# Kernel optimization log

Hardware: AMD Instinct MI355X
Metric: run time of the kernel (lower is better)

Reference implementation:

```python
import jax, jax.numpy as jnp
import numpy as np

B, T, C, H = 2, 2048, 1024, 16
D = C // H  # 64
RW, RA, RG = 64, 64, 128  # decay / a / gate LoRA ranks
EPS = 1e-5


def setup_inputs() -> dict:
    key = jax.random.key(0)
    ks = iter(jax.random.split(key, 40))
    n = lambda s, sc=0.02: jax.random.normal(next(ks), s, jnp.float32) * sc
    u = lambda s: jax.random.uniform(next(ks), s, jnp.float32)
    return dict(
        hidden_states=jax.random.normal(next(ks), (B, T, C), jnp.float32),
        # token-mix (time-shift lerp) params
        x_r=u((C,)), x_w=u((C,)), x_k=u((C,)), x_v=u((C,)), x_a=u((C,)), x_g=u((C,)),
        k_k=u((C,)), k_a=u((C,)), r_k=n((H, D), 0.1),
        # square projections (stored [in, out]; x @ W)
        W_r=n((C, C)), W_k=n((C, C)), W_v=n((C, C)), W_o=n((C, C)),
        # LoRA: out = act(x @ A) @ Bm + bias (activation between the two linears)
        w_lora_a=n((C, RW)), w_lora_b=n((RW, C)), w_lora_bias=n((C,), 0.1),
        a_lora_a=n((C, RA)), a_lora_b=n((RA, C)), a_lora_bias=jnp.zeros((C,), jnp.float32),
        g_lora_a=n((C, RG)), g_lora_b=n((RG, C)), g_lora_bias=jnp.zeros((C,), jnp.float32),
        # GroupNorm(num_heads groups over value_dim)
        gn_weight=jnp.ones((C,), jnp.float32), gn_bias=jnp.zeros((C,), jnp.float32),
    )


def _rwkv7_scan(r, log_w, k, v, a, b):
    # all inputs [B, T, H, D]; state S: [B, H, D_v, D_k]
    # S_t = S_{t-1} * diag(exp(log_w_t)) + (S_{t-1} @ a_t) b_t^T + v_t k_t^T
    # o_t = S_t @ r_t
    Bn, Tn, Hn, Dn = r.shape

    def step(S, xs):
        r_t, w_t, k_t, v_t, a_t, b_t = xs  # each [B, H, D]
        sa = jnp.einsum('bhij,bhj->bhi', S, a_t)          # S @ a (pre-decay state)
        S = (S * jnp.exp(w_t)[:, :, None, :]
             + sa[..., None] * b_t[:, :, None, :]
             + v_t[..., None] * k_t[:, :, None, :])
        o_t = jnp.einsum('bhij,bhj->bhi', S, r_t)
        return S, o_t

    S0 = jnp.zeros((Bn, Hn, Dn, Dn), r.dtype)
    xs = tuple(jnp.swapaxes(x, 0, 1) for x in (r, log_w, k, v, a, b))  # [T,B,H,D]
    _, o = jax.lax.scan(step, S0, xs)
    return jnp.swapaxes(o, 0, 1)  # [B, T, H, D]


def reference(hidden_states, x_r, x_w, x_k, x_v, x_a, x_g, k_k, k_a, r_k,
              W_r, W_k, W_v, W_o,
              w_lora_a, w_lora_b, w_lora_bias,
              a_lora_a, a_lora_b, a_lora_bias,
              g_lora_a, g_lora_b, g_lora_bias,
              gn_weight, gn_bias):
    Bn, Tn, Cn = hidden_states.shape
    # time shift: pad one step of zeros at the front, drop last
    shifted = jnp.concatenate([jnp.zeros_like(hidden_states[:, :1]), hidden_states[:, :-1]], axis=1)
    delta = shifted - hidden_states

    xr = hidden_states + delta * x_r
    xw = hidden_states + delta * x_w
    xk = hidden_states + delta * x_k
    xv = hidden_states + delta * x_v
    xa = hidden_states + delta * x_a

    r = xr @ W_r
    log_w = -jax.nn.softplus(-((jnp.tanh(xw @ w_lora_a) @ w_lora_b) + w_lora_bias)) - 0.5
    k = xk @ W_k
    v = xv @ W_v
    a = jax.nn.sigmoid((xa @ a_lora_a) @ a_lora_b + a_lora_bias)
    # g_lora(r): sigmoid activation sits BETWEEN the two LoRA linears
    g = jax.nn.sigmoid(r @ g_lora_a) @ g_lora_b + g_lora_bias

    kk = (k * k_k).reshape(Bn, Tn, H, D)
    kk = kk / jnp.maximum(jnp.linalg.norm(kk, axis=-1, keepdims=True), 1e-12)  # per-head L2 norm
    k = k * (1.0 + (a - 1.0) * k_a)

    rh = r.reshape(Bn, Tn, H, D)
    wh = log_w.reshape(Bn, Tn, H, D)
    kh = k.reshape(Bn, Tn, H, D)
    vh = v.reshape(Bn, Tn, H, D)
    ah = a.reshape(Bn, Tn, H, D)

    o = _rwkv7_scan(rh, wh, kh, vh, -kk, kk * ah)  # [B, T, H, D]

    # GroupNorm over value_dim with H groups (stats per head)
    mu = o.mean(-1, keepdims=True)
    var = ((o - mu) ** 2).mean(-1, keepdims=True)
    o_flat = ((o - mu) * jax.lax.rsqrt(var + EPS)).reshape(Bn, Tn, C) * gn_weight + gn_bias

    bonus = ((rh * kh * r_k).sum(-1, keepdims=True) * vh).reshape(Bn, Tn, C)
    o_flat = o_flat + bonus
    return (o_flat * g) @ W_o
```

## Files before the change

### kernel.cpp

```cpp
#include <hip/hip_runtime.h>
#include <hip/hip_bf16.h>
#include <hip/hip_fp16.h>
#include <stdint.h>
#include <stddef.h>

typedef __hip_bfloat16 bf16;
typedef _Float16 f16;
typedef __attribute__((ext_vector_type(8))) short short8;
typedef __attribute__((ext_vector_type(8))) _Float16 half8;
typedef __attribute__((ext_vector_type(4))) float f32x4;
typedef __attribute__((ext_vector_type(2))) float f32x2;
typedef unsigned short us;

__device__ __forceinline__ float dsigm(float z){ return 1.f/(1.f+expf(-z)); }

template<int CTRL>
__device__ __forceinline__ float dpp_term(float x) {
  int xi = __builtin_bit_cast(int, x);
  int yi = __builtin_amdgcn_update_dpp(0, xi, CTRL, 0xF, 0xF, false);
  return __builtin_bit_cast(float, yi);
}
__device__ __forceinline__ float red4(float x) {
  x += dpp_term<0xB1>(x);
  x += dpp_term<0x4E>(x);
  return x;
}

__device__ __forceinline__ void split1(float v, us& h, us& l) {
  bf16 hb = __float2bfloat16(v);
  h = __builtin_bit_cast(us, hb);
  float hf = __bfloat162float(hb);
  bf16 lb = __float2bfloat16(v - hf);
  l = __builtin_bit_cast(us, lb);
}

__device__ __forceinline__ void split8(const float* f, short8& h, short8& l) {
#pragma unroll
  for (int e = 0; e < 8; ++e) {
    us hh, ll;
    split1(f[e], hh, ll);
    h[e] = (short)hh; l[e] = (short)ll;
  }
}

__device__ __forceinline__ void gl16(const f16* g, f16* l) {
  __builtin_amdgcn_global_load_lds((const __attribute__((address_space(1))) void*)g,
                                   (__attribute__((address_space(3))) void*)l, 16, 0, 0);
}

__device__ __forceinline__ void emit16(const float* __restrict__ marr, int c4,
    const float4& cur, const float4& dlt, f16* __restrict__ out, int row)
{
  float4 m = *(const float4*)(marr + c4);
  f16* o = out + (size_t)row*1024 + c4;
  o[0] = (f16)fmaf(dlt.x, m.x, cur.x);
  o[1] = (f16)fmaf(dlt.y, m.y, cur.y);
  o[2] = (f16)fmaf(dlt.z, m.z, cur.z);
  o[3] = (f16)fmaf(dlt.w, m.w, cur.w);
}

__global__ void k_prep(const float* __restrict__ hs,
    const float* __restrict__ mr, const float* __restrict__ mw, const float* __restrict__ mk,
    const float* __restrict__ mv, const float* __restrict__ ma,
    f16* __restrict__ oxr, f16* __restrict__ oxw, f16* __restrict__ oxk,
    f16* __restrict__ oxv, f16* __restrict__ oxa)
{
  int id = blockIdx.x * 256 + threadIdx.x;
  int row = id >> 8;
  int c4 = (id & 255) << 2;
  int t = row & 2047;
  const float* hp = hs + (size_t)row*1024 + c4;
  float4 cur = *(const float4*)hp;
  float4 prev = make_float4(0.f,0.f,0.f,0.f);
  if (t > 0) prev = *(const float4*)(hp - 1024);
  float4 dlt = make_float4(prev.x-cur.x, prev.y-cur.y, prev.z-cur.z, prev.w-cur.w);
  emit16(mr, c4, cur, dlt, oxr, row);
  emit16(mw, c4, cur, dlt, oxw, row);
  emit16(mk, c4, cur, dlt, oxk, row);
  emit16(mv, c4, cur, dlt, oxv, row);
  emit16(ma, c4, cur, dlt, oxa, row);
}

struct SrcP { const float* p[10]; };
struct DstP { f16* p[10]; };

__global__ void k_transpose(SrcP S, DstP Dd)
{
  static constexpr int TR[10]  = {1024,1024,1024,1024,1024,  64,1024,  64,1024, 128};
  static constexpr int TCC[10] = {1024,1024,1024,1024,  64,1024,  64,1024, 128,1024};
  static constexpr int TCP[10] = {1024,1024,1024,1024, 128,1024, 128,1024, 128,1024};
  int z = blockIdx.z;
  int R = TR[z], Cc = TCC[z], Cp = TCP[z];
  int n0 = blockIdx.x * 32, r0 = blockIdx.y * 32;
  if (n0 >= Cp || r0 >= R) return;
  const float* src = S.p[z];
  f16* dst = Dd.p[z];
  int tx = threadIdx.x, ty = threadIdx.y;
  __shared__ float tile[32][33];
  if (n0 < Cc) {
#pragma unroll
    for (int i = 0; i < 4; ++i)
      tile[ty + 8*i][tx] = src[(size_t)(r0 + ty + 8*i)*Cc + n0 + tx];
    __syncthreads();
#pragma unroll
    for (int i = 0; i < 4; ++i)
      dst[(size_t)(n0 + ty + 8*i)*R + r0 + tx] = (f16)tile[tx][ty + 8*i];
  } else {
#pragma unroll
    for (int i = 0; i < 4; ++i)
      dst[(size_t)(n0 + ty + 8*i)*R + r0 + tx] = (f16)0.f;
  }
}

struct GJob {
  const f16* A;
  const f16* Bt;
  float* C;
  f16* Cpk;
  const float* bias;
  int K; int N; int Npk; int ldc; int act;
  int lda; int ldb;
};
struct GJobs { GJob j[5]; };

__global__ __launch_bounds__(256) void k_gemm_fp16(GJobs jobs)
{
  GJob jb = jobs.j[blockIdx.z];
  const int colBase = blockIdx.y * 128;
  if (colBase >= jb.N) return;
  const int rowBase = blockIdx.x * 128;
  __shared__ __align__(16) f16 As[128*64];
  __shared__ __align__(16) f16 Bs[128*64];
  const int tid = threadIdx.x;
  const int l = tid & 63, w = tid >> 6;
  const int wm = w >> 1, wn = w & 1;
  const int lrow = l & 15;
  const int nk = jb.K >> 6;

  const f16* Arow[4]; const f16* Brow[4]; int ld[4];
#pragma unroll
  for (int i2 = 0; i2 < 4; ++i2) {
    int s = (i2*4 + w)*64 + l;
    int ar = s >> 3;
    int unit = s & 7;
    int acs = (unit ^ (ar & 7)) * 8;
    Arow[i2] = jb.A  + (size_t)(rowBase + ar)*jb.lda + acs;
    Brow[i2] = jb.Bt + (size_t)(colBase + ar)*jb.ldb + acs;
    ld[i2] = (i2*4 + w) * 512;
  }

  f32x4 acc[4][4];
#pragma unroll
  for (int i = 0; i < 4; ++i)
#pragma unroll
    for (int j = 0; j < 4; ++j) { f32x4 z = {0.f,0.f,0.f,0.f}; acc[i][j] = z; }

  for (int kt = 0; kt < nk; ++kt) {
    const int kh = kt*64;
#pragma unroll
    for (int i2 = 0; i2 < 4; ++i2) {
      gl16(Arow[i2] + kh, &As[ld[i2]]);
      gl16(Brow[i2] + kh, &Bs[ld[i2]]);
    }
    __syncthreads();
#pragma unroll
    for (int ks = 0; ks < 2; ++ks) {
      half8 ah[4], bh[4];
#pragma unroll
      for (int mt = 0; mt < 4; ++mt) {
        int row = wm*64 + mt*16 + lrow;
        int cu = ks*4 + (l >> 4);
        ah[mt] = *(const half8*)&As[row*64 + ((cu ^ (row & 7)) * 8)];
      }
#pragma unroll
      for (int nt = 0; nt < 4; ++nt) {
        int row = wn*64 + nt*16 + lrow;
        int cu = ks*4 + (l >> 4);
        bh[nt] = *(const half8*)&Bs[row*64 + ((cu ^ (row & 7)) * 8)];
      }
#pragma unroll
      for (int mt = 0; mt < 4; ++mt)
#pragma unroll
        for (int nt = 0; nt < 4; ++nt)
          acc[mt][nt] = __builtin_amdgcn_mfma_f32_16x16x32_f16(ah[mt], bh[nt], acc[mt][nt], 0, 0, 0);
    }
    __syncthreads();
  }
#pragma unroll
  for (int mt = 0; mt < 4; ++mt) {
    int row = rowBase + wm*64 + mt*16 + (l >> 4)*4;
#pragma unroll
    for (int nt = 0; nt < 4; ++nt) {
      int col = colBase + wn*64 + nt*16 + (l & 15);
      float bv = (jb.bias != nullptr) ? jb.bias[col] : 0.f;
#pragma unroll
      for (int rg = 0; rg < 4; ++rg) {
        float v = acc[mt][nt][rg] + bv;
        if (jb.act == 1)      v = dsigm(v);
        else if (jb.act == 2) v = tanhf(v);
        else if (jb.act == 3) v = 0.60653066f * dsigm(v);
        if (jb.C) jb.C[(size_t)(row + rg)*jb.ldc + col] = v;
        if (jb.Cpk && col < jb.Npk)
          jb.Cpk[(size_t)(row + rg)*jb.Npk + col] = (f16)v;
      }
    }
  }
}

__global__ void k_scanprep(f16* __restrict__ kA, f16* __restrict__ aA,
                           const float* __restrict__ kkw, const float* __restrict__ kaw,
                           f16* __restrict__ kkA)
{
  int idx = blockIdx.x * 256 + threadIdx.x;
  size_t gt8 = (size_t)idx * 8;
  int ch = (int)(gt8 & 1023);
  half8 k8 = *(const half8*)(kA + gt8);
  half8 a8 = *(const half8*)(aA + gt8);
  float kw[8], ka_[8];
  *(float4*)&kw[0]  = *(const float4*)(kkw + ch);
  *(float4*)&kw[4]  = *(const float4*)(kkw + ch + 4);
  *(float4*)&ka_[0] = *(const float4*)(kaw + ch);
  *(float4*)&ka_[4] = *(const float4*)(kaw + ch + 4);
  float kkv[8]; float ss = 0.f;
#pragma unroll
  for (int e = 0; e < 8; ++e) { kkv[e] = (float)k8[e] * kw[e]; ss += kkv[e]*kkv[e]; }
  ss += __shfl_xor(ss, 1); ss += __shfl_xor(ss, 2); ss += __shfl_xor(ss, 4);
  float inv = 1.f / fmaxf(sqrtf(ss), 1e-12f);
  half8 kkn8, bb8, kup8;
#pragma unroll
  for (int e = 0; e < 8; ++e) {
    float kkn = kkv[e] * inv;
    float av = (float)a8[e];
    kkn8[e] = (f16)kkn;
    bb8[e]  = (f16)(kkn * av);
    kup8[e] = (f16)((float)k8[e] * fmaf(av - 1.f, ka_[e], 1.f));
  }
  *(half8*)(kkA + gt8) = kkn8;
  *(half8*)(aA + gt8)  = bb8;
  *(half8*)(kA + gt8)  = kup8;
}

__device__ __forceinline__ void step_pk16(const float* __restrict__ sb, int s,
    f32x2* u2, f32x2* p2, float* __restrict__ o0A, float* __restrict__ zA,
    size_t base, int i, int q, int j0)
{
  f32x2 kk2[8];
#pragma unroll
  for (int hh = 0; hh < 4; ++hh) {
    float4 a1 = *(const float4*)(sb + 512 + s*64 + j0 + hh*4);
    kk2[hh*2+0] = f32x2{a1.x, a1.y}; kk2[hh*2+1] = f32x2{a1.z, a1.w};
  }
  f32x2 uk2 = u2[0]*kk2[0], pk2 = p2[0]*kk2[0];
#pragma unroll
  for (int e = 1; e < 8; ++e) { uk2 += u2[e]*kk2[e]; pk2 += p2[e]*kk2[e]; }
  float uk = red4(uk2.x + uk2.y);
  float pk = red4(pk2.x + pk2.y);
  float vi = sb[2560 + s*64 + i];
  const f32x2 su2 = {-uk, -uk}, sp2 = {-pk, -pk}, vi2 = {vi, vi};
  f32x2 oo2 = {0.f, 0.f}, zz2 = {0.f, 0.f};
#pragma unroll
  for (int hh = 0; hh < 4; ++hh) {
    float4 e4 = *(const float4*)(sb + 0    + s*64 + j0 + hh*4);
    float4 b4 = *(const float4*)(sb + 1024 + s*64 + j0 + hh*4);
    float4 k4 = *(const float4*)(sb + 1536 + s*64 + j0 + hh*4);
    float4 r4 = *(const float4*)(sb + 2048 + s*64 + j0 + hh*4);
    f32x2 ew0 = {e4.x, e4.y}, ew1 = {e4.z, e4.w};
    f32x2 bb0 = {b4.x, b4.y}, bb1 = {b4.z, b4.w};
    f32x2 kv0 = {k4.x, k4.y}, kv1 = {k4.z, k4.w};
    f32x2 rr0 = {r4.x, r4.y}, rr1 = {r4.z, r4.w};
    int e0 = hh*2, e1 = hh*2 + 1;
    f32x2 uu0 = u2[e0]*ew0 + su2*bb0 + vi2*kv0;
    u2[e0] = uu0; oo2 += uu0*rr0;
    f32x2 pp0 = p2[e0]*ew0 + sp2*bb0;
    p2[e0] = pp0; zz2 += pp0*rr0;
    f32x2 uu1 = u2[e1]*ew1 + su2*bb1 + vi2*kv1;
    u2[e1] = uu1; oo2 += uu1*rr1;
    f32x2 pp1 = p2[e1]*ew1 + sp2*bb1;
    p2[e1] = pp1; zz2 += pp1*rr1;
  }
  float oo = red4(oo2.x + oo2.y);
  float zz = red4(zz2.x + zz2.y);
  if (q == 0) { o0A[base + i] = oo; zA[base + i] = zz; }
}

__global__ __launch_bounds__(256) void k_scan_p1(
    const f16* __restrict__ rA, const f16* __restrict__ ewA,
    const f16* __restrict__ kA, const f16* __restrict__ vA,
    const f16* __restrict__ kkA, const f16* __restrict__ bbA,
    float* __restrict__ o0A, float* __restrict__ zA,
    float* __restrict__ UcA, float* __restrict__ PTcA)
{
  const int blk = blockIdx.x;
  const int bh = blk & 31, c = blk >> 5;
  const int b = bh >> 4, h = bh & 15;
  const int tid = threadIdx.x;
  const int i = tid >> 2, q = tid & 3, j0 = q * 16;
  const size_t base0 = (size_t)b*2048*1024 + (size_t)h*64 + (size_t)(c*64)*1024;

  __shared__ __align__(16) float smem[6144];

  const int aA_ = tid >> 6, rmA = tid & 63, ssA = rmA >> 3, fA = rmA & 7;
  const f16* paA = (aA_==0) ? ewA : (aA_==1) ? kkA : (aA_==2) ? bbA : kA;
  const f16* srcA = paA + base0 + (size_t)ssA*1024 + fA*8;
  const int dstA = aA_*512 + ssA*64 + fA*8;
  const int hasB = (tid < 128);
  const int sB = 256 + tid;
  const int aB_ = sB >> 6, rmB = sB & 63, ssB = rmB >> 3, fB = rmB & 7;
  const f16* paB = (aB_ == 4) ? rA : vA;
  const f16* srcB = paB + base0 + (size_t)ssB*1024 + fB*8;
  const int dstB = aB_*512 + ssB*64 + fB*8;

  f32x2 u2[8], p2[8];
#pragma unroll
  for (int e = 0; e < 8; ++e) {
    u2[e] = f32x2{0.f, 0.f};
    float p0 = (j0 + 2*e     == i) ? 1.f : 0.f;
    float p1 = (j0 + 2*e + 1 == i) ? 1.f : 0.f;
    p2[e] = f32x2{p0, p1};
  }

  {
    half8 hA = *(const half8*)(srcA);
    *(float4*)&smem[dstA]     = make_float4((float)hA[0], (float)hA[1], (float)hA[2], (float)hA[3]);
    *(float4*)&smem[dstA + 4] = make_float4((float)hA[4], (float)hA[5], (float)hA[6], (float)hA[7]);
    if (hasB) {
      half8 hB = *(const half8*)(srcB);
      *(float4*)&smem[dstB]     = make_float4((float)hB[0], (float)hB[1], (float)hB[2], (float)hB[3]);
      *(float4*)&smem[dstB + 4] = make_float4((float)hB[4], (float)hB[5], (float)hB[6], (float)hB[7]);
    }
  }
  __syncthreads();

  int curb = 0;
  for (int g = 0; g < 8; ++g) {
    half8 nA, nB;
    if (g < 7) {
      nA = *(const half8*)(srcA + (size_t)(g+1)*8192);
      if (hasB) nB = *(const half8*)(srcB + (size_t)(g+1)*8192);
    }
    const float* sb = smem + curb*3072;
#pragma unroll
    for (int s = 0; s < 8; ++s)
      step_pk16(sb, s, u2, p2, o0A, zA, base0 + (size_t)(g*8 + s)*1024, i, q, j0);
    if (g < 7) {
      int nb = curb ^ 1;
      *(float4*)&smem[nb*3072 + dstA]     = make_float4((float)nA[0], (float)nA[1], (float)nA[2], (float)nA[3]);
      *(float4*)&smem[nb*3072 + dstA + 4] = make_float4((float)nA[4], (float)nA[5], (float)nA[6], (float)nA[7]);
      if (hasB) {
        *(float4*)&smem[nb*3072 + dstB]     = make_float4((float)nB[0], (float)nB[1], (float)nB[2], (float)nB[3]);
        *(float4*)&smem[nb*3072 + dstB + 4] = make_float4((float)nB[4], (float)nB[5], (float)nB[6], (float)nB[7]);
      }
    }
    __syncthreads();
    curb ^= 1;
  }

  const size_t cbase = ((size_t)(bh*32 + c)) * 4096;
#pragma unroll
  for (int e4 = 0; e4 < 4; ++e4)
    *(float4*)(UcA + cbase + (size_t)i*64 + j0 + e4*4) =
      make_float4(u2[e4*2].x, u2[e4*2].y, u2[e4*2+1].x, u2[e4*2+1].y);
  float (*lds)[65] = (float(*)[65])smem;
#pragma unroll
  for (int e = 0; e < 8; ++e) {
    lds[i][j0 + 2*e]     = p2[e].x;
    lds[i][j0 + 2*e + 1] = p2[e].y;
  }
  __syncthreads();
#pragma unroll
  for (int e4 = 0; e4 < 4; ++e4) {
    float4 wv = make_float4(lds[j0 + e4*4 + 0][i], lds[j0 + e4*4 + 1][i],
                            lds[j0 + e4*4 + 2][i], lds[j0 + e4*4 + 3][i]);
    *(float4*)(PTcA + cbase + (size_t)i*64 + j0 + e4*4) = wv;
  }
}

__device__ __forceinline__ void chain_body(int c, int bh, int w, int lr, int lq,
    float (&Slds)[64][65], f32x4 (&acc)[4],
    float (&u_c)[4][4], float4 (&p_c)[2][2],
    float (&u_n)[4][4], float4 (&p_n)[2][2],
    const float* __restrict__ UcA, const float* __restrict__ PTcA,
    float* __restrict__ S0A)
{
  const size_t s0base = ((size_t)bh*32 + c) * 4096;
#pragma unroll
  for (int mt = 0; mt < 4; ++mt)
#pragma unroll
    for (int rg = 0; rg < 4; ++rg) {
      Slds[mt*16 + lq*4 + rg][w*16 + lr] = acc[mt][rg];
      if (c > 0) S0A[s0base + (size_t)(mt*16 + lq*4 + rg)*64 + w*16 + lr] = acc[mt][rg];
    }
  __syncthreads();
  if (c + 1 < 32) {
    const size_t nbase = ((size_t)bh*32 + c + 1) * 4096;
#pragma unroll
    for (int mt = 0; mt < 4; ++mt)
#pragma unroll
      for (int rg = 0; rg < 4; ++rg)
        u_n[mt][rg] = UcA[nbase + (size_t)(mt*16 + lq*4 + rg)*64 + w*16 + lr];
#pragma unroll
    for (int kt = 0; kt < 2; ++kt)
#pragma unroll
      for (int hh = 0; hh < 2; ++hh)
        p_n[kt][hh] = *(const float4*)(PTcA + nbase + (size_t)(w*16 + lr)*64 + kt*32 + lq*8 + hh*4);
  }
  short8 pbh[2], pbl[2];
#pragma unroll
  for (int kt = 0; kt < 2; ++kt) {
    float f[8] = {p_c[kt][0].x, p_c[kt][0].y, p_c[kt][0].z, p_c[kt][0].w,
                  p_c[kt][1].x, p_c[kt][1].y, p_c[kt][1].z, p_c[kt][1].w};
    split8(f, pbh[kt], pbl[kt]);
  }
  f32x4 nacc[4];
#pragma unroll
  for (int mt = 0; mt < 4; ++mt) {
    f32x4 z = {u_c[mt][0], u_c[mt][1], u_c[mt][2], u_c[mt][3]};
    nacc[mt] = z;
  }
#pragma unroll
  for (int kt = 0; kt < 2; ++kt)
#pragma unroll
    for (int mt = 0; mt < 4; ++mt) {
      float f[8];
#pragma unroll
      for (int e = 0; e < 8; ++e) f[e] = Slds[mt*16 + lr][kt*32 + lq*8 + e];
      short8 sah, sal;
      split8(f, sah, sal);
      nacc[mt] = __builtin_amdgcn_mfma_f32_16x16x32_bf16(sah, pbh[kt], nacc[mt], 0, 0, 0);
      nacc[mt] = __builtin_amdgcn_mfma_f32_16x16x32_bf16(sal, pbh[kt], nacc[mt], 0, 0, 0);
      nacc[mt] = __builtin_amdgcn_mfma_f32_16x16x32_bf16(sah, pbl[kt], nacc[mt], 0, 0, 0);
    }
#pragma unroll
  for (int mt = 0; mt < 4; ++mt) acc[mt] = nacc[mt];
  __syncthreads();
}

__global__ __launch_bounds__(256) void k_chain(
    const float* __restrict__ UcA, const float* __restrict__ PTcA,
    float* __restrict__ S0A)
{
  const int bh = blockIdx.x;
  const int l = threadIdx.x & 63, w = threadIdx.x >> 6;
  const int lr = l & 15, lq = l >> 4;
  __shared__ float Slds[64][65];

  f32x4 acc[4];
#pragma unroll
  for (int mt = 0; mt < 4; ++mt) { f32x4 z = {0.f,0.f,0.f,0.f}; acc[mt] = z; }

  float u0[4][4], u1[4][4];
  float4 p0[2][2], p1[2][2];
  {
    const size_t cbase = (size_t)bh * 32 * 4096;
#pragma unroll
    for (int mt = 0; mt < 4; ++mt)
#pragma unroll
      for (int rg = 0; rg < 4; ++rg)
        u0[mt][rg] = UcA[cbase + (size_t)(mt*16 + lq*4 + rg)*64 + w*16 + lr];
#pragma unroll
    for (int kt = 0; kt < 2; ++kt)
#pragma unroll
      for (int hh = 0; hh < 2; ++hh)
        p0[kt][hh] = *(const float4*)(PTcA + cbase + (size_t)(w*16 + lr)*64 + kt*32 + lq*8 + hh*4);
  }
  for (int c = 0; c < 32; c += 2) {
    chain_body(c,     bh, w, lr, lq, Slds, acc, u0, p0, u1, p1, UcA, PTcA, S0A);
    chain_body(c + 1, bh, w, lr, lq, Slds, acc, u1, p1, u0, p0, UcA, PTcA, S0A);
  }
}

__global__ __launch_bounds__(256) void k_corrpost(
    const float* __restrict__ S0A, const float* __restrict__ zA,
    const float* __restrict__ o0A, const f16* __restrict__ rA,
    const f16* __restrict__ kA, const f16* __restrict__ vA,
    const float* __restrict__ rk, const float* __restrict__ gnw,
    const float* __restrict__ gnb, const f16* __restrict__ gA,
    f16* __restrict__ yH)
{
  const int blk = blockIdx.x;
  const int bh = blk & 31;
  const int c  = blk >> 5;
  const int b = bh >> 4, h = bh & 15;
  const int l = threadIdx.x & 63, w = threadIdx.x >> 6;
  const int lr = l & 15, lq = l >> 4;

  f32x4 a2[4];
#pragma unroll
  for (int nt = 0; nt < 4; ++nt) { f32x4 z = {0.f,0.f,0.f,0.f}; a2[nt] = z; }

  if (c > 0) {
    const size_t s0base = ((size_t)bh*32 + c) * 4096;
    short8 sbh[4][2], sbl[4][2];
#pragma unroll
    for (int nt = 0; nt < 4; ++nt)
#pragma unroll
      for (int kt = 0; kt < 2; ++kt) {
        float f[8];
#pragma unroll
        for (int e = 0; e < 8; ++e)
          f[e] = S0A[s0base + (size_t)(nt*16 + lr)*64 + kt*32 + lq*8 + e];
        split8(f, sbh[nt][kt], sbl[nt][kt]);
      }
    short8 zh[2], zl[2];
#pragma unroll
    for (int kt = 0; kt < 2; ++kt) {
      const float* zp = zA + ((size_t)(b*2048 + c*64 + w*16 + lr)*16 + h)*64 + kt*32 + lq*8;
      float f[8];
#pragma unroll
      for (int e = 0; e < 8; ++e) f[e] = zp[e];
      split8(f, zh[kt], zl[kt]);
    }
#pragma unroll
    for (int kt = 0; kt < 2; ++kt)
#pragma unroll
      for (int nt = 0; nt < 4; ++nt) {
        a2[nt] = __builtin_amdgcn_mfma_f32_16x16x32_bf16(zh[kt], sbh[nt][kt], a2[nt], 0, 0, 0);
        a2[nt] = __builtin_amdgcn_mfma_f32_16x16x32_bf16(zl[kt], sbh[nt][kt], a2[nt], 0, 0, 0);
        a2[nt] = __builtin_amdgcn_mfma_f32_16x16x32_bf16(zh[kt], sbl[nt][kt], a2[nt], 0, 0, 0);
      }
  }

#pragma unroll
  for (int rg = 0; rg < 4; ++rg) {
    const int tl = w*16 + lq*4 + rg;
    const size_t trow = (size_t)(b*2048 + c*64 + tl);
    const size_t rb = trow*1024 + h*64;
    float o4[4], v4[4];
    float sum = 0.f, pr = 0.f;
#pragma unroll
    for (int nt = 0; nt < 4; ++nt) {
      const int ii = nt*16 + lr;
      float o = o0A[rb + ii] + a2[nt][rg];
      o4[nt] = o; sum += o;
      v4[nt] = (float)vA[rb + ii];
      pr += (float)rA[rb + ii] * (float)kA[rb + ii] * rk[h*64 + ii];
    }
    sum += __shfl_xor(sum,1); sum += __shfl_xor(sum,2);
    sum += __shfl_xor(sum,4); sum += __shfl_xor(sum,8);
    pr  += __shfl_xor(pr,1);  pr  += __shfl_xor(pr,2);
    pr  += __shfl_xor(pr,4);  pr  += __shfl_xor(pr,8);
    float mean = sum * (1.f/64.f);
    float vp = 0.f;
#pragma unroll
    for (int nt = 0; nt < 4; ++nt) { float d = o4[nt]-mean; vp += d*d; }
    vp += __shfl_xor(vp,1); vp += __shfl_xor(vp,2);
    vp += __shfl_xor(vp,4); vp += __shfl_xor(vp,8);
    float inv = rsqrtf(vp*(1.f/64.f) + 1e-5f);
#pragma unroll
    for (int nt = 0; nt < 4; ++nt) {
      const int ii = nt*16 + lr;
      const int ch = h*64 + ii;
      float y = (o4[nt]-mean)*inv*gnw[ch] + gnb[ch];
      y = fmaf(pr, v4[nt], y);
      y *= (float)gA[rb + ii];
      yH[trow*1024 + ch] = (f16)y;
    }
  }
}

extern "C" void kernel_launch(void* const* d_in, const int* in_sizes, int n_in,
                              void* d_out, int out_size, void* d_ws, size_t ws_size,
                              hipStream_t stream)
{
  (void)in_sizes; (void)n_in; (void)out_size; (void)ws_size;
  const float* hs     = (const float*)d_in[0];
  const float* x_r    = (const float*)d_in[1];
  const float* x_w    = (const float*)d_in[2];
  const float* x_k    = (const float*)d_in[3];
  const float* x_v    = (const float*)d_in[4];
  const float* x_a    = (const float*)d_in[5];
  const float* k_k    = (const float*)d_in[7];
  const float* k_a    = (const float*)d_in[8];
  const float* r_k    = (const float*)d_in[9];
  const float* W_r    = (const float*)d_in[10];
  const float* W_k    = (const float*)d_in[11];
  const float* W_v    = (const float*)d_in[12];
  const float* W_o    = (const float*)d_in[13];
  const float* wla    = (const float*)d_in[14];
  const float* wlb    = (const float*)d_in[15];
  const float* wlbias = (const float*)d_in[16];
  const float* ala    = (const float*)d_in[17];
  const float* alb    = (const float*)d_in[18];
  const float* albias = (const float*)d_in[19];
  const float* gla    = (const float*)d_in[20];
  const float* glb    = (const float*)d_in[21];
  const float* glbias = (const float*)d_in[22];
  const float* gnw    = (const float*)d_in[23];
  const float* gnb    = (const float*)d_in[24];

  char* ws = (char*)d_ws;
  size_t cur = 0;
  auto take = [&](size_t bytes) { size_t o = cur; cur += (bytes + 255) & ~(size_t)255; return o; };

  f16* xr_h = (f16*)(ws + take((size_t)4096*1024*2));
  f16* xw_h = (f16*)(ws + take((size_t)4096*1024*2));
  f16* xk_h = (f16*)(ws + take((size_t)4096*1024*2));
  f16* xv_h = (f16*)(ws + take((size_t)4096*1024*2));
  f16* xa_h = (f16*)(ws + take((size_t)4096*1024*2));
  f16* Wr_p  = (f16*)(ws + take((size_t)1024*1024*2));
  f16* Wk_p  = (f16*)(ws + take((size_t)1024*1024*2));
  f16* Wv_p  = (f16*)(ws + take((size_t)1024*1024*2));
  f16* Wo_p  = (f16*)(ws + take((size_t)1024*1024*2));
  f16* wla_p = (f16*)(ws + take((size_t)128*1024*2));
  f16* wlb_p = (f16*)(ws + take((size_t)1024*64*2));
  f16* ala_p = (f16*)(ws + take((size_t)128*1024*2));
  f16* alb_p = (f16*)(ws + take((size_t)1024*64*2));
  f16* gla_p = (f16*)(ws + take((size_t)128*1024*2));
  f16* glb_p = (f16*)(ws + take((size_t)1024*128*2));
  f16* r_h  = (f16*)(ws + take((size_t)4096*1024*2));
  f16* k_h  = (f16*)(ws + take((size_t)4096*1024*2));
  f16* v_h  = (f16*)(ws + take((size_t)4096*1024*2));
  f16* kk_h = (f16*)(ws + take((size_t)4096*1024*2));
  f16* g_h  = (f16*)(ws + take((size_t)4096*1024*2));
  f16* t2w  = (f16*)(ws + take((size_t)4096*64*2));
  f16* t2a  = (f16*)(ws + take((size_t)4096*64*2));
  f16* t2g  = (f16*)(ws + take((size_t)4096*128*2));
  float* z_f  = (float*)(ws + take((size_t)4096*1024*4));
  float* Uc_f = (float*)(ws + take((size_t)4096*1024*4));
  float* PT_f = (float*)(ws + take((size_t)4096*1024*4));
  f16*   ew_h = xw_h;
  f16*   a_h  = xa_h;
  f16*   y_h  = xr_h;
  float* S0_f = (float*)xk_h;
  float* oF   = (float*)d_out;

  k_prep<<<4096, 256, 0, stream>>>(hs, x_r, x_w, x_k, x_v, x_a,
                                   xr_h, xw_h, xk_h, xv_h, xa_h);
  SrcP sp; DstP dp;
  sp.p[0]=W_r; sp.p[1]=W_k; sp.p[2]=W_v; sp.p[3]=W_o;
  sp.p[4]=wla; sp.p[5]=wlb; sp.p[6]=ala; sp.p[7]=alb; sp.p[8]=gla; sp.p[9]=glb;
  dp.p[0]=Wr_p; dp.p[1]=Wk_p; dp.p[2]=Wv_p; dp.p[3]=Wo_p;
  dp.p[4]=wla_p; dp.p[5]=wlb_p; dp.p[6]=ala_p; dp.p[7]=alb_p; dp.p[8]=gla_p; dp.p[9]=glb_p;
  k_transpose<<<dim3(32,32,10), dim3(32,8), 0, stream>>>(sp, dp);

  GJobs J{};
  auto job = [](const f16* A, const f16* Bt, float* C, f16* Cpk, const float* bias,
                int K, int N, int Npk, int ldc, int act, int lda, int ldb) {
    GJob j; j.A=A; j.Bt=Bt; j.C=C; j.Cpk=Cpk; j.bias=bias;
    j.K=K; j.N=N; j.Npk=Npk; j.ldc=ldc; j.act=act; j.lda=lda; j.ldb=ldb;
    return j;
  };

  J.j[0] = job(xr_h, Wr_p,  nullptr, r_h, nullptr, 1024, 1024, 1024, 0, 0, 1024, 1024);
  J.j[1] = job(xk_h, Wk_p,  nullptr, k_h, nullptr, 1024, 1024, 1024, 0, 0, 1024, 1024);
  J.j[2] = job(xv_h, Wv_p,  nullptr, v_h, nullptr, 1024, 1024, 1024, 0, 0, 1024, 1024);
  J.j[3] = job(xw_h, wla_p, nullptr, t2w, nullptr, 1024, 128,  64,   0, 2, 1024, 1024);
  J.j[4] = job(xa_h, ala_p, nullptr, t2a, nullptr, 1024, 128,  64,   0, 0, 1024, 1024);
  k_gemm_fp16<<<dim3(32,8,5), 256, 0, stream>>>(J);

  J = GJobs{};
  J.j[0] = job(t2w, wlb_p, nullptr, ew_h, wlbias, 64,   1024, 1024, 0, 3, 64,   64);
  J.j[1] = job(t2a, alb_p, nullptr, a_h,  albias, 64,   1024, 1024, 0, 1, 64,   64);
  J.j[2] = job(r_h, gla_p, nullptr, t2g,  nullptr, 1024, 128,  128,  0, 1, 1024, 1024);
  k_gemm_fp16<<<dim3(32,8,3), 256, 0, stream>>>(J);

  J = GJobs{};
  J.j[0] = job(t2g, glb_p, nullptr, g_h, glbias, 128, 1024, 1024, 0, 0, 128, 128);
  k_gemm_fp16<<<dim3(32,8,1), 256, 0, stream>>>(J);

  k_scanprep<<<2048, 256, 0, stream>>>(k_h, a_h, k_k, k_a, kk_h);

  k_scan_p1<<<1024, 256, 0, stream>>>(r_h, ew_h, k_h, v_h, kk_h, a_h, oF, z_f, Uc_f, PT_f);
  k_chain<<<32, 256, 0, stream>>>(Uc_f, PT_f, S0_f);

  k_corrpost<<<1024, 256, 0, stream>>>(S0_f, z_f, oF, r_h, k_h, v_h,
                                       r_k, gnw, gnb, g_h, y_h);

  J = GJobs{};
  J.j[0] = job(y_h, Wo_p, (float*)d_out, nullptr, nullptr, 1024, 1024, 0, 1024, 0, 1024, 1024);
  k_gemm_fp16<<<dim3(32,8,1), 256, 0, stream>>>(J);
}
```

Before: 315.4 us.

## Split chunk scan into separate U and P state blocks for more parallelism

The first-phase chunked scan kernel used to advance both the zero-init state U and the identity-init transition P in one block. It now launches twice as many blocks, each advancing only one of the two recurrences, with smaller staged tiles of 4 timesteps and a smaller shared-memory footprint. The aim is more concurrent blocks and fewer registers per thread, which improves occupancy and latency hiding on the serial recurrence. The cost is that shared inputs (ew, kk, bb, r) are loaded twice, and there are more sync rounds per chunk.

```diff
diff --git a/kernel.cpp b/kernel.cpp
--- a/kernel.cpp
+++ b/kernel.cpp
@@ -240,30 +240,28 @@
   *(half8*)(kA + gt8)  = kup8;
 }
 
-__device__ __forceinline__ void step_pk16(const float* __restrict__ sb, int s,
-    f32x2* u2, f32x2* p2, float* __restrict__ o0A, float* __restrict__ zA,
-    size_t base, int i, int q, int j0)
+__device__ __forceinline__ void step_U(const float* __restrict__ sb, int s,
+    f32x2* u2, float* __restrict__ o0A, size_t base, int i, int q, int j0)
 {
   f32x2 kk2[8];
 #pragma unroll
   for (int hh = 0; hh < 4; ++hh) {
-    float4 a1 = *(const float4*)(sb + 512 + s*64 + j0 + hh*4);
+    float4 a1 = *(const float4*)(sb + 256 + s*64 + j0 + hh*4);
     kk2[hh*2+0] = f32x2{a1.x, a1.y}; kk2[hh*2+1] = f32x2{a1.z, a1.w};
   }
-  f32x2 uk2 = u2[0]*kk2[0], pk2 = p2[0]*kk2[0];
-#pragma unroll
-  for (int e = 1; e < 8; ++e) { uk2 += u2[e]*kk2[e]; pk2 += p2[e]*kk2[e]; }
+  f32x2 uk2 = u2[0]*kk2[0];
+#pragma unroll
+  for (int e = 1; e < 8; ++e) uk2 += u2[e]*kk2[e];
   float uk = red4(uk2.x + uk2.y);
-  float pk = red4(pk2.x + pk2.y);
-  float vi = sb[2560 + s*64 + i];
-  const f32x2 su2 = {-uk, -uk}, sp2 = {-pk, -pk}, vi2 = {vi, vi};
-  f32x2 oo2 = {0.f, 0.f}, zz2 = {0.f, 0.f};
+  float vi = sb[1280 + s*64 + i];
+  const f32x2 su2 = {-uk, -uk}, vi2 = {vi, vi};
+  f32x2 oo2 = {0.f, 0.f};
 #pragma unroll
   for (int hh = 0; hh < 4; ++hh) {
     float4 e4 = *(const float4*)(sb + 0    + s*64 + j0 + hh*4);
-    float4 b4 = *(const float4*)(sb + 1024 + s*64 + j0 + hh*4);
-    float4 k4 = *(const float4*)(sb + 1536 + s*64 + j0 + hh*4);
-    float4 r4 = *(const float4*)(sb + 2048 + s*64 + j0 + hh*4);
+    float4 b4 = *(const float4*)(sb + 512  + s*64 + j0 + hh*4);
+    float4 k4 = *(const float4*)(sb + 768  + s*64 + j0 + hh*4);
+    float4 r4 = *(const float4*)(sb + 1024 + s*64 + j0 + hh*4);
     f32x2 ew0 = {e4.x, e4.y}, ew1 = {e4.z, e4.w};
     f32x2 bb0 = {b4.x, b4.y}, bb1 = {b4.z, b4.w};
     f32x2 kv0 = {k4.x, k4.y}, kv1 = {k4.z, k4.w};
@@ -271,16 +269,44 @@
     int e0 = hh*2, e1 = hh*2 + 1;
     f32x2 uu0 = u2[e0]*ew0 + su2*bb0 + vi2*kv0;
     u2[e0] = uu0; oo2 += uu0*rr0;
+    f32x2 uu1 = u2[e1]*ew1 + su2*bb1 + vi2*kv1;
+    u2[e1] = uu1; oo2 += uu1*rr1;
+  }
+  float oo = red4(oo2.x + oo2.y);
+  if (q == 0) o0A[base + i] = oo;
+}
+
+__device__ __forceinline__ void step_P(const float* __restrict__ sb, int s,
+    f32x2* p2, float* __restrict__ zA, size_t base, int i, int q, int j0)
+{
+  f32x2 kk2[8];
+#pragma unroll
+  for (int hh = 0; hh < 4; ++hh) {
+    float4 a1 = *(const float4*)(sb + 256 + s*64 + j0 + hh*4);
+    kk2[hh*2+0] = f32x2{a1.x, a1.y}; kk2[hh*2+1] = f32x2{a1.z, a1.w};
+  }
+  f32x2 pk2 = p2[0]*kk2[0];
+#pragma unroll
+  for (int e = 1; e < 8; ++e) pk2 += p2[e]*kk2[e];
+  float pk = red4(pk2.x + pk2.y);
+  const f32x2 sp2 = {-pk, -pk};
+  f32x2 zz2 = {0.f, 0.f};
+#pragma unroll
+  for (int hh = 0; hh < 4; ++hh) {
+    float4 e4 = *(const float4*)(sb + 0   + s*64 + j0 + hh*4);
+    float4 b4 = *(const float4*)(sb + 512 + s*64 + j0 + hh*4);
+    float4 r4 = *(const float4*)(sb + 768 + s*64 + j0 + hh*4);
+    f32x2 ew0 = {e4.x, e4.y}, ew1 = {e4.z, e4.w};
+    f32x2 bb0 = {b4.x, b4.y}, bb1 = {b4.z, b4.w};
+    f32x2 rr0 = {r4.x, r4.y}, rr1 = {r4.z, r4.w};
+    int e0 = hh*2, e1 = hh*2 + 1;
     f32x2 pp0 = p2[e0]*ew0 + sp2*bb0;
     p2[e0] = pp0; zz2 += pp0*rr0;
-    f32x2 uu1 = u2[e1]*ew1 + su2*bb1 + vi2*kv1;
-    u2[e1] = uu1; oo2 += uu1*rr1;
     f32x2 pp1 = p2[e1]*ew1 + sp2*bb1;
     p2[e1] = pp1; zz2 += pp1*rr1;
   }
-  float oo = red4(oo2.x + oo2.y);
   float zz = red4(zz2.x + zz2.y);
-  if (q == 0) { o0A[base + i] = oo; zA[base + i] = zz; }
+  if (q == 0) zA[base + i] = zz;
 }
 
 __global__ __launch_bounds__(256) void k_scan_p1(
@@ -291,87 +317,89 @@
     float* __restrict__ UcA, float* __restrict__ PTcA)
 {
   const int blk = blockIdx.x;
-  const int bh = blk & 31, c = blk >> 5;
+  const int role = blk >> 10;
+  const int idx = blk & 1023;
+  const int bh = idx & 31, c = idx >> 5;
   const int b = bh >> 4, h = bh & 15;
   const int tid = threadIdx.x;
   const int i = tid >> 2, q = tid & 3, j0 = q * 16;
   const size_t base0 = (size_t)b*2048*1024 + (size_t)h*64 + (size_t)(c*64)*1024;
 
-  __shared__ __align__(16) float smem[6144];
-
-  const int aA_ = tid >> 6, rmA = tid & 63, ssA = rmA >> 3, fA = rmA & 7;
-  const f16* paA = (aA_==0) ? ewA : (aA_==1) ? kkA : (aA_==2) ? bbA : kA;
-  const f16* srcA = paA + base0 + (size_t)ssA*1024 + fA*8;
-  const int dstA = aA_*512 + ssA*64 + fA*8;
-  const int hasB = (tid < 128);
-  const int sB = 256 + tid;
-  const int aB_ = sB >> 6, rmB = sB & 63, ssB = rmB >> 3, fB = rmB & 7;
-  const f16* paB = (aB_ == 4) ? rA : vA;
-  const f16* srcB = paB + base0 + (size_t)ssB*1024 + fB*8;
-  const int dstB = aB_*512 + ssB*64 + fB*8;
-
-  f32x2 u2[8], p2[8];
+  __shared__ __align__(16) float smem[4160];
+
+  const int nslots = role ? 128 : 192;
+  const int a0 = tid >> 5, rm = tid & 31, s0 = rm >> 3, f0 = rm & 7;
+  const f16* pa;
+  if (role == 0)
+    pa = (a0==0) ? ewA : (a0==1) ? kkA : (a0==2) ? bbA :
+         (a0==3) ? kA  : (a0==4) ? rA  : vA;
+  else
+    pa = (a0==0) ? ewA : (a0==1) ? kkA : (a0==2) ? bbA : rA;
+  const int active = (tid < nslots);
+  const f16* src0 = pa + base0 + (size_t)s0*1024 + f0*8;
+  const int dst0 = a0*256 + s0*64 + f0*8;
+
+  f32x2 st[8];
 #pragma unroll
   for (int e = 0; e < 8; ++e) {
-    u2[e] = f32x2{0.f, 0.f};
-    float p0 = (j0 + 2*e     == i) ? 1.f : 0.f;
-    float p1 = (j0 + 2*e + 1 == i) ? 1.f : 0.f;
-    p2[e] = f32x2{p0, p1};
-  }
-
-  {
-    half8 hA = *(const half8*)(srcA);
-    *(float4*)&smem[dstA]     = make_float4((float)hA[0], (float)hA[1], (float)hA[2], (float)hA[3]);
-    *(float4*)&smem[dstA + 4] = make_float4((float)hA[4], (float)hA[5], (float)hA[6], (float)hA[7]);
-    if (hasB) {
-      half8 hB = *(const half8*)(srcB);
-      *(float4*)&smem[dstB]     = make_float4((float)hB[0], (float)hB[1], (float)hB[2], (float)hB[3]);
-      *(float4*)&smem[dstB + 4] = make_float4((float)hB[4], (float)hB[5], (float)hB[6], (float)hB[7]);
-    }
+    if (role == 0) st[e] = f32x2{0.f, 0.f};
+    else {
+      float p0 = (j0 + 2*e     == i) ? 1.f : 0.f;
+      float p1 = (j0 + 2*e + 1 == i) ? 1.f : 0.f;
+      st[e] = f32x2{p0, p1};
+    }
+  }
+
+  if (active) {
+    half8 hh = *(const half8*)(src0);
+    *(float4*)&smem[dst0]     = make_float4((float)hh[0], (float)hh[1], (float)hh[2], (float)hh[3]);
+    *(float4*)&smem[dst0 + 4] = make_float4((float)hh[4], (float)hh[5], (float)hh[6], (float)hh[7]);
   }
   __syncthreads();
 
   int curb = 0;
-  for (int g = 0; g < 8; ++g) {
-    half8 nA, nB;
-    if (g < 7) {
-      nA = *(const half8*)(srcA + (size_t)(g+1)*8192);
-      if (hasB) nB = *(const half8*)(srcB + (size_t)(g+1)*8192);
-    }
-    const float* sb = smem + curb*3072;
-#pragma unroll
-    for (int s = 0; s < 8; ++s)
-      step_pk16(sb, s, u2, p2, o0A, zA, base0 + (size_t)(g*8 + s)*1024, i, q, j0);
-    if (g < 7) {
+  for (int g = 0; g < 16; ++g) {
+    half8 n0;
+    if (g < 15 && active) n0 = *(const half8*)(src0 + (size_t)(g+1)*4096);
+    const float* sb = smem + curb*1536;
+    if (role == 0) {
+#pragma unroll
+      for (int s = 0; s < 4; ++s)
+        step_U(sb, s, st, o0A, base0 + (size_t)(g*4 + s)*1024, i, q, j0);
+    } else {
+#pragma unroll
+      for (int s = 0; s < 4; ++s)
+        step_P(sb, s, st, zA, base0 + (size_t)(g*4 + s)*1024, i, q, j0);
+    }
+    if (g < 15 && active) {
       int nb = curb ^ 1;
-      *(float4*)&smem[nb*3072 + dstA]     = make_float4((float)nA[0], (float)nA[1], (float)nA[2], (float)nA[3]);
-      *(float4*)&smem[nb*3072 + dstA + 4] = make_float4((float)nA[4], (float)nA[5], (float)nA[6], (float)nA[7]);
-      if (hasB) {
-        *(float4*)&smem[nb*3072 + dstB]     = make_float4((float)nB[0], (float)nB[1], (float)nB[2], (float)nB[3]);
-        *(float4*)&smem[nb*3072 + dstB + 4] = make_float4((float)nB[4], (float)nB[5], (float)nB[6], (float)nB[7]);
-      }
+      *(float4*)&smem[nb*1536 + dst0]     = make_float4((float)n0[0], (float)n0[1], (float)n0[2], (float)n0[3]);
+      *(float4*)&smem[nb*1536 + dst0 + 4] = make_float4((float)n0[4], (float)n0[5], (float)n0[6], (float)n0[7]);
     }
     __syncthreads();
     curb ^= 1;
   }
 
   const size_t cbase = ((size_t)(bh*32 + c)) * 4096;
-#pragma unroll
-  for (int e4 = 0; e4 < 4; ++e4)
-    *(float4*)(UcA + cbase + (size_t)i*64 + j0 + e4*4) =
-      make_float4(u2[e4*2].x, u2[e4*2].y, u2[e4*2+1].x, u2[e4*2+1].y);
-  float (*lds)[65] = (float(*)[65])smem;
-#pragma unroll
-  for (int e = 0; e < 8; ++e) {
-    lds[i][j0 + 2*e]     = p2[e].x;
-    lds[i][j0 + 2*e + 1] = p2[e].y;
-  }
-  __syncthreads();
-#pragma unroll
-  for (int e4 = 0; e4 < 4; ++e4) {
-    float4 wv = make_float4(lds[j0 + e4*4 + 0][i], lds[j0 + e4*4 + 1][i],
-                            lds[j0 + e4*4 + 2][i], lds[j0 + e4*4 + 3][i]);
-    *(float4*)(PTcA + cbase + (size_t)i*64 + j0 + e4*4) = wv;
+  if (role == 0) {
+#pragma unroll
+    for (int e4 = 0; e4 < 4; ++e4)
+      *(float4*)(UcA + cbase + (size_t)i*64 + j0 + e4*4) =
+        make_float4(st[e4*2].x, st[e4*2].y, st[e4*2+1].x, st[e4*2+1].y);
+  } else {
+    float (*lds)[65] = (float(*)[65])smem;
+#pragma unroll
+    for (int e = 0; e < 8; ++e) {
+      lds[i][j0 + 2*e]     = st[e].x;
+      lds[i][j0 + 2*e + 1] = st[e].y;
+    }
+    __syncthreads();
+#pragma unroll
+    for (int e4 = 0; e4 < 4; ++e4) {
+      float4 wv = make_float4(lds[j0 + e4*4 + 0][i], lds[j0 + e4*4 + 1][i],
+                              lds[j0 + e4*4 + 2][i], lds[j0 + e4*4 + 3][i]);
+      *(float4*)(PTcA + cbase + (size_t)i*64 + j0 + e4*4) = wv;
+    }
   }
 }
 
@@ -660,7 +688,7 @@
 
   k_scanprep<<<2048, 256, 0, stream>>>(k_h, a_h, k_k, k_a, kk_h);
 
-  k_scan_p1<<<1024, 256, 0, stream>>>(r_h, ew_h, k_h, v_h, kk_h, a_h, oF, z_f, Uc_f, PT_f);
+  k_scan_p1<<<2048, 256, 0, stream>>>(r_h, ew_h, k_h, v_h, kk_h, a_h, oF, z_f, Uc_f, PT_f);
   k_chain<<<32, 256, 0, stream>>>(Uc_f, PT_f, S0_f);
 
   k_corrpost<<<1024, 256, 0, stream>>>(S0_f, z_f, oF, r_h, k_h, v_h,
```

Result: slower. 338.0 us (+7.2%).
